# Optimization experiments

Measured on AMD Instinct MI355X. Metric: run time of the kernel, lower is better.

## Reference

```python
import jax, jax.numpy as jnp
import numpy as np

EPS = 1e-05


def setup_inputs() -> dict:
    key = jax.random.key(0)
    ks = jax.random.split(key, 7)
    N, C_in, H, W = 32, 64, 128, 128
    C_out, K = 128, 3
    x = jax.random.normal(ks[0], (N, C_in, H, W), dtype=jnp.float32)
    weight = jax.random.normal(ks[1], (C_out, C_in, K, K), dtype=jnp.float32) * 0.05
    bias = jax.random.normal(ks[2], (C_out,), dtype=jnp.float32) * 0.1
    gamma = jax.random.uniform(ks[3], (C_out,), dtype=jnp.float32, minval=0.5, maxval=1.5)
    beta = jax.random.normal(ks[4], (C_out,), dtype=jnp.float32) * 0.1
    running_mean = jax.random.normal(ks[5], (C_out,), dtype=jnp.float32) * 0.1
    running_var = jax.random.uniform(ks[6], (C_out,), dtype=jnp.float32, minval=0.5, maxval=1.5)
    return {"x": x, "weight": weight, "bias": bias, "gamma": gamma,
            "beta": beta, "running_mean": running_mean, "running_var": running_var}


def reference(x, weight, bias, gamma, beta, running_mean, running_var):
    # conv2d, stride=1, VALID padding, NCHW / OIHW
    z = jax.lax.conv_general_dilated(
        x, weight, window_strides=(1, 1), padding='VALID',
        dimension_numbers=('NCHW', 'OIHW', 'NCHW'))
    z = z + bias[None, :, None, None]
    # mish-like: z * tanh(softplus(z))
    z = z * jnp.tanh(jax.nn.softplus(z))
    # BatchNorm inference folded to per-channel affine
    scale = gamma / jnp.sqrt(running_var + EPS)
    shift = beta - running_mean * scale
    return z * scale[None, :, None, None] + shift[None, :, None, None]
```

## Files before the change

kernel.cpp:

```cpp
#include <hip/hip_runtime.h>

typedef unsigned int  u32;
typedef unsigned short u16;
typedef __attribute__((ext_vector_type(8))) short short8;
typedef __attribute__((ext_vector_type(4))) float f32x4;

#define CI 64
#define CO 128
#define HH 128
#define WW 128
#define HO 126
#define WO 126

__device__ __forceinline__ u16 f2bf(float f) {
    u32 u = __builtin_bit_cast(u32, f);
    u = (u + 0x7FFFu + ((u >> 16) & 1u)) >> 16;
    return (u16)u;
}

__global__ void reorder_w(const float* __restrict__ w, u16* __restrict__ wq) {
    int i = blockIdx.x * 256 + threadIdx.x;
    if (i < 9 * CO * CI) {
        int ci  = i & 63;
        int co  = (i >> 6) & 127;
        int tap = i >> 13;
        wq[i] = f2bf(w[(co * CI + ci) * 9 + tap]);
    }
}

__global__ __launch_bounds__(256, 2)
void conv_mfma(const float* __restrict__ x, const u16* __restrict__ wq,
               const float* __restrict__ bias, const float* __restrict__ gamma,
               const float* __restrict__ beta, const float* __restrict__ rmean,
               const float* __restrict__ rvar, float* __restrict__ out) {
    __shared__ u32 in_lds[3 * 130 * 32];
    __shared__ float s_scale[CO], s_shift[CO], s_bias[CO];

    const int tid = threadIdx.x;
    const int h0  = blockIdx.x;
    const int n   = blockIdx.y;

    if (tid < CO) {
        float sc = gamma[tid] * rsqrtf(rvar[tid] + 1e-5f);
        s_scale[tid] = sc;
        s_shift[tid] = beta[tid] - rmean[tid] * sc;
        s_bias[tid]  = bias[tid];
    }
    if (tid < 48) {
        int kh  = tid >> 4;
        int rem = tid & 15;
        int w   = 128 + (rem & 1);
        int g   = rem >> 1;
        uint4 z = {0u, 0u, 0u, 0u};
        *(uint4*)&in_lds[(kh * 130 + w) * 32 + ((g ^ (w & 7)) * 4)] = z;
    }
    const float* xb = x + (size_t)n * CI * HH * WW;
    for (int it = 0; it < 12; ++it) {
        int idx = it * 256 + tid;
        int w   = idx & 127;
        int g   = (idx >> 7) & 7;
        int kh  = idx >> 10;
        const float* p = xb + (g * 8) * (HH * WW) + (h0 + kh) * WW + w;
        float v[8];
#pragma unroll
        for (int j = 0; j < 8; ++j) v[j] = p[j * (HH * WW)];
        uint4 q;
        q.x = (u32)f2bf(v[0]) | ((u32)f2bf(v[1]) << 16);
        q.y = (u32)f2bf(v[2]) | ((u32)f2bf(v[3]) << 16);
        q.z = (u32)f2bf(v[4]) | ((u32)f2bf(v[5]) << 16);
        q.w = (u32)f2bf(v[6]) | ((u32)f2bf(v[7]) << 16);
        *(uint4*)&in_lds[(kh * 130 + w) * 32 + ((g ^ (w & 7)) * 4)] = q;
    }
    __syncthreads();

    const int wv = tid >> 6;
    const int li = tid & 15;
    const int qd = (tid & 63) >> 4;
    const int wm = wv & 1;
    const int wn = wv >> 1;

    f32x4 zero4 = {0.f, 0.f, 0.f, 0.f};
    f32x4 acc[4][4];
#pragma unroll
    for (int i = 0; i < 4; ++i)
#pragma unroll
        for (int j = 0; j < 4; ++j) acc[i][j] = zero4;

    const uint4* wg = (const uint4*)wq;

#pragma unroll 1
    for (int kh = 0; kh < 3; ++kh) {
#pragma unroll
        for (int kw = 0; kw < 3; ++kw) {
            const int tap = kh * 3 + kw;
#pragma unroll
            for (int ks = 0; ks < 2; ++ks) {
                short8 a[4], b[4];
#pragma unroll
                for (int i = 0; i < 4; ++i) {
                    int co = wm * 64 + i * 16 + li;
                    a[i] = __builtin_bit_cast(short8,
                        wg[tap * 1024 + co * 8 + ks * 4 + qd]);
                }
#pragma unroll
                for (int j = 0; j < 4; ++j) {
                    int w = wn * 64 + j * 16 + li + kw;
                    int g = ks * 4 + qd;
                    b[j] = *(const short8*)&in_lds[(kh * 130 + w) * 32 +
                                                   ((g ^ (w & 7)) * 4)];
                }
#pragma unroll
                for (int i = 0; i < 4; ++i)
#pragma unroll
                    for (int j = 0; j < 4; ++j)
                        acc[i][j] = __builtin_amdgcn_mfma_f32_16x16x32_bf16(
                            a[i], b[j], acc[i][j], 0, 0, 0);
            }
        }
    }

    float* ob = out + (size_t)n * CO * (HO * WO) + (size_t)h0 * WO;
#pragma unroll
    for (int j = 0; j < 4; ++j) {
        int wo = wn * 64 + j * 16 + li;
        if (wo < WO) {
#pragma unroll
            for (int i = 0; i < 4; ++i) {
#pragma unroll
                for (int r = 0; r < 4; ++r) {
                    int co  = wm * 64 + i * 16 + qd * 4 + r;
                    float z = acc[i][j][r] + s_bias[co];
                    float zc = fminf(z, 20.0f);
                    float u  = 1.0f + __expf(zc);
                    float u2 = u * u;
                    float t  = (u2 - 1.0f) / (u2 + 1.0f);
                    ob[(size_t)co * (HO * WO) + wo] = z * t * s_scale[co] + s_shift[co];
                }
            }
        }
    }
}

extern "C" void kernel_launch(void* const* d_in, const int* in_sizes, int n_in,
                              void* d_out, int out_size, void* d_ws, size_t ws_size,
                              hipStream_t stream) {
    const float* x     = (const float*)d_in[0];
    const float* wt    = (const float*)d_in[1];
    const float* bias  = (const float*)d_in[2];
    const float* gamma = (const float*)d_in[3];
    const float* beta  = (const float*)d_in[4];
    const float* rmean = (const float*)d_in[5];
    const float* rvar  = (const float*)d_in[6];
    u16* wq = (u16*)d_ws;

    hipLaunchKernelGGL(reorder_w, dim3(288), dim3(256), 0, stream, wt, wq);
    hipLaunchKernelGGL(conv_mfma, dim3(HO, 32), dim3(256), 0, stream,
                       x, wq, bias, gamma, beta, rmean, rvar, (float*)d_out);
}
```

Measured before the change: 574.9 us.

## Pre-convert input to swizzled bf16 buffer and stream rows via direct-to-LDS loads

Adds a prep kernel that converts x once to bf16 in a per-row channel-last, XOR-swizzled layout in workspace. The conv kernel then fills LDS with async global_load_lds copies instead of reconverting each input row three times with strided fp32 loads. This removes redundant conversion and the stride-HxW gathers, but adds an extra pass that writes and rereads a 64 MB intermediate, and it needs enough workspace or falls back to the old path. The epilogue division also switches to the fast __fdividef.

```diff
diff --git a/kernel.cpp b/kernel.cpp
--- a/kernel.cpp
+++ b/kernel.cpp
@@ -25,6 +25,129 @@
         int co  = (i >> 6) & 127;
         int tap = i >> 13;
         wq[i] = f2bf(w[(co * CI + ci) * 9 + tap]);
+    }
+}
+
+__global__ __launch_bounds__(256)
+void prep_x(const float* __restrict__ x, u16* __restrict__ xq) {
+    const int row = blockIdx.x;
+    const int n = row >> 7, h = row & 127;
+    const float* xb = x + (size_t)n * CI * HH * WW + (size_t)h * WW;
+    u16* dst = xq + (size_t)row * 8192;
+    for (int it = 0; it < 4; ++it) {
+        int idx  = it * 256 + threadIdx.x;
+        int slot = idx & 7;
+        int w    = idx >> 3;
+        int g    = slot ^ (w & 7);
+        const float* p = xb + (g * 8) * (HH * WW) + w;
+        float v[8];
+#pragma unroll
+        for (int j = 0; j < 8; ++j) v[j] = p[j * (HH * WW)];
+        uint4 q;
+        q.x = (u32)f2bf(v[0]) | ((u32)f2bf(v[1]) << 16);
+        q.y = (u32)f2bf(v[2]) | ((u32)f2bf(v[3]) << 16);
+        q.z = (u32)f2bf(v[4]) | ((u32)f2bf(v[5]) << 16);
+        q.w = (u32)f2bf(v[6]) | ((u32)f2bf(v[7]) << 16);
+        *(uint4*)(dst + (size_t)w * 64 + slot * 8) = q;
+    }
+}
+
+__global__ __launch_bounds__(256, 2)
+void conv_mfma_v2(const u16* __restrict__ xq, const u16* __restrict__ wq,
+                  const float* __restrict__ bias, const float* __restrict__ gamma,
+                  const float* __restrict__ beta, const float* __restrict__ rmean,
+                  const float* __restrict__ rvar, float* __restrict__ out) {
+    __shared__ u16 in_lds[3 * 128 * 64];
+    __shared__ float s_scale[CO], s_shift[CO], s_bias[CO];
+
+    const int tid = threadIdx.x;
+    const int h0  = blockIdx.x;
+    const int n   = blockIdx.y;
+
+    if (tid < CO) {
+        float sc = gamma[tid] * rsqrtf(rvar[tid] + 1e-5f);
+        s_scale[tid] = sc;
+        s_shift[tid] = beta[tid] - rmean[tid] * sc;
+        s_bias[tid]  = bias[tid];
+    }
+
+    const int wv   = tid >> 6;
+    const int lane = tid & 63;
+    const u16* src = xq + (size_t)(n * 128 + h0) * 8192;
+#pragma unroll
+    for (int s = 0; s < 12; ++s) {
+        int chunk = s * 4 + wv;
+        const u16* gp = src + chunk * 512 + lane * 8;
+        u16*       lp = in_lds + chunk * 512 + lane * 8;
+        __builtin_amdgcn_global_load_lds(
+            (const __attribute__((address_space(1))) u32*)gp,
+            (__attribute__((address_space(3))) u32*)lp, 16, 0, 0);
+    }
+    __syncthreads();
+
+    const int li = tid & 15;
+    const int qd = (tid & 63) >> 4;
+    const int wm = wv & 1;
+    const int wn = wv >> 1;
+
+    f32x4 zero4 = {0.f, 0.f, 0.f, 0.f};
+    f32x4 acc[4][4];
+#pragma unroll
+    for (int i = 0; i < 4; ++i)
+#pragma unroll
+        for (int j = 0; j < 4; ++j) acc[i][j] = zero4;
+
+    const uint4* wg = (const uint4*)wq;
+
+#pragma unroll 1
+    for (int kh = 0; kh < 3; ++kh) {
+#pragma unroll
+        for (int kw = 0; kw < 3; ++kw) {
+            const int tap = kh * 3 + kw;
+#pragma unroll
+            for (int ks = 0; ks < 2; ++ks) {
+                short8 a[4], b[4];
+#pragma unroll
+                for (int i = 0; i < 4; ++i) {
+                    int co = wm * 64 + i * 16 + li;
+                    a[i] = __builtin_bit_cast(short8,
+                        wg[tap * 1024 + co * 8 + ks * 4 + qd]);
+                }
+#pragma unroll
+                for (int j = 0; j < 4; ++j) {
+                    int w = wn * 64 + j * 16 + li + kw;
+                    int g = ks * 4 + qd;
+                    b[j] = *(const short8*)&in_lds[(size_t)(kh * 128 + w) * 64 +
+                                                   ((g ^ (w & 7)) * 8)];
+                }
+#pragma unroll
+                for (int i = 0; i < 4; ++i)
+#pragma unroll
+                    for (int j = 0; j < 4; ++j)
+                        acc[i][j] = __builtin_amdgcn_mfma_f32_16x16x32_bf16(
+                            a[i], b[j], acc[i][j], 0, 0, 0);
+            }
+        }
+    }
+
+    float* ob = out + (size_t)n * CO * (HO * WO) + (size_t)h0 * WO;
+#pragma unroll
+    for (int j = 0; j < 4; ++j) {
+        int wo = wn * 64 + j * 16 + li;
+        if (wo < WO) {
+#pragma unroll
+            for (int i = 0; i < 4; ++i) {
+#pragma unroll
+                for (int r = 0; r < 4; ++r) {
+                    int co  = wm * 64 + i * 16 + qd * 4 + r;
+                    float z  = acc[i][j][r] + s_bias[co];
+                    float u  = 1.0f + __expf(fminf(z, 20.0f));
+                    float u2 = u * u;
+                    float t  = __fdividef(u2 - 1.0f, u2 + 1.0f);
+                    ob[(size_t)co * (HO * WO) + wo] = z * t * s_scale[co] + s_shift[co];
+                }
+            }
+        }
     }
 }
 
@@ -129,11 +252,10 @@
 #pragma unroll
                 for (int r = 0; r < 4; ++r) {
                     int co  = wm * 64 + i * 16 + qd * 4 + r;
-                    float z = acc[i][j][r] + s_bias[co];
-                    float zc = fminf(z, 20.0f);
-                    float u  = 1.0f + __expf(zc);
+                    float z  = acc[i][j][r] + s_bias[co];
+                    float u  = 1.0f + __expf(fminf(z, 20.0f));
                     float u2 = u * u;
-                    float t  = (u2 - 1.0f) / (u2 + 1.0f);
+                    float t  = __fdividef(u2 - 1.0f, u2 + 1.0f);
                     ob[(size_t)co * (HO * WO) + wo] = z * t * s_scale[co] + s_shift[co];
                 }
             }
@@ -151,9 +273,21 @@
     const float* beta  = (const float*)d_in[4];
     const float* rmean = (const float*)d_in[5];
     const float* rvar  = (const float*)d_in[6];
-    u16* wq = (u16*)d_ws;
-
-    hipLaunchKernelGGL(reorder_w, dim3(288), dim3(256), 0, stream, wt, wq);
-    hipLaunchKernelGGL(conv_mfma, dim3(HO, 32), dim3(256), 0, stream,
-                       x, wq, bias, gamma, beta, rmean, rvar, (float*)d_out);
-}
+
+    const size_t XQ_BYTES = (size_t)64 * 1024 * 1024;
+    const size_t WQ_BYTES = (size_t)9 * CO * CI * 2;
+
+    if (ws_size >= XQ_BYTES + WQ_BYTES) {
+        u16* xq = (u16*)d_ws;
+        u16* wq = (u16*)((char*)d_ws + XQ_BYTES);
+        hipLaunchKernelGGL(reorder_w, dim3(288), dim3(256), 0, stream, wt, wq);
+        hipLaunchKernelGGL(prep_x, dim3(4096), dim3(256), 0, stream, x, xq);
+        hipLaunchKernelGGL(conv_mfma_v2, dim3(HO, 32), dim3(256), 0, stream,
+                           xq, wq, bias, gamma, beta, rmean, rvar, (float*)d_out);
+    } else {
+        u16* wq = (u16*)d_ws;
+        hipLaunchKernelGGL(reorder_w, dim3(288), dim3(256), 0, stream, wt, wq);
+        hipLaunchKernelGGL(conv_mfma, dim3(HO, 32), dim3(256), 0, stream,
+                           x, wq, bias, gamma, beta, rmean, rvar, (float*)d_out);
+    }
+}
```

New measurement: 569.8 us. No clear change (-0.9%).
